# Kernel optimization log

Hardware: AMD Instinct MI355X
Metric: run time of the kernel (lower is better)

Reference implementation:

```python
import jax, jax.numpy as jnp
import numpy as np

V, MAXLEN, D, I, C, L, S = 32000, 4096, 1024, 4096, 1024, 4, 4096


def setup_inputs() -> dict:
    key = jax.random.key(0)
    ks = jax.random.split(key, 20)
    sd = 0.02
    inp = {
        "input_indices": jax.random.randint(ks[0], (S,), 0, V),
        "emb": jax.random.normal(ks[1], (V, D), jnp.float32) * sd,
        "pos": jax.random.normal(ks[2], (MAXLEN, D), jnp.float32) * sd,
        "Wq": jax.random.normal(ks[3], (L, D, I), jnp.float32) * sd,
        "bq": jnp.zeros((L, I), jnp.float32),
        "Wk": jax.random.normal(ks[4], (L, D, I), jnp.float32) * sd,
        "bk": jnp.zeros((L, I), jnp.float32),
        "Wv": jax.random.normal(ks[5], (L, D, I), jnp.float32) * sd,
        "bv": jnp.zeros((L, I), jnp.float32),
        "Wo": jax.random.normal(ks[6], (L, I, D), jnp.float32) * sd,
        "bo": jnp.zeros((L, D), jnp.float32),
        "W1": jax.random.normal(ks[7], (L, D, I), jnp.float32) * sd,
        "b1": jnp.zeros((L, I), jnp.float32),
        "W2": jax.random.normal(ks[8], (L, I, D), jnp.float32) * sd,
        "b2": jnp.zeros((L, D), jnp.float32),
        "Wout": jax.random.normal(ks[9], (D, C), jnp.float32) * sd,
        "bout": jnp.zeros((C,), jnp.float32),
    }
    return inp


def reference(input_indices, emb, pos, Wq, bq, Wk, bk, Wv, bv, Wo, bo, W1, b1, W2, b2, Wout, bout):
    s = input_indices.shape[0]
    x = emb[input_indices] + pos[:s]  # [S, D]
    causal_mask = jnp.triu(jnp.ones((s, s), bool), k=1)  # True above diagonal -> masked
    scale = 1.0 / np.sqrt(Wq.shape[-1]).astype(np.float32)

    def layer(x, p):
        wq, bq_, wk, bk_, wv, bv_, wo, bo_, w1, b1_, w2, b2_ = p
        q = x @ wq + bq_  # [S, I]
        k = x @ wk + bk_
        v = x @ wv + bv_
        scores = (q @ k.T) * scale  # [S, S]
        scores = jnp.where(causal_mask, -jnp.inf, scores)
        attn = jax.nn.softmax(scores, axis=-1)
        r = x + (attn @ v) @ wo + bo_  # residual + attention output projection
        f = jnp.maximum(r @ w1 + b1_, 0.0) @ w2 + b2_  # ReLU FFN
        return r + f, attn

    x, attention_maps = jax.lax.scan(
        layer, x, (Wq, bq, Wk, bk, Wv, bv, Wo, bo, W1, b1, W2, b2)
    )
    logits = x @ Wout + bout  # [S, C]
    log_probs = jax.nn.log_softmax(logits, axis=-1)
    return log_probs, attention_maps  # [S, C], [L, S, S]
```

## Files before the change

kernel.cpp:

```cpp
#include <hip/hip_runtime.h>
#include <stdint.h>
#include <math.h>

#define S_ 4096
#define D_ 1024
#define I_ 4096
#define C_ 1024
#define L_ 4

typedef unsigned short u16;
typedef short bf16x8 __attribute__((ext_vector_type(8)));
typedef float f32x4 __attribute__((ext_vector_type(4)));

__device__ __forceinline__ u16 f2bf(float f) {
  union { float f; uint32_t u; } c; c.f = f;
  return (u16)((c.u + 0x7FFFu + ((c.u >> 16) & 1u)) >> 16);
}
__device__ __forceinline__ float bf2f(u16 b) {
  union { uint32_t u; float f; } c; c.u = (uint32_t)b << 16;
  return c.f;
}
__device__ __forceinline__ u16 f2h(float f) {
  _Float16 h = (_Float16)f;
  return *(u16*)&h;
}
__device__ __forceinline__ float h2f(u16 b) {
  _Float16 h = *(_Float16*)&b;
  return (float)h;
}

__device__ __forceinline__ void gll16(const void* g, void* l) {
  __builtin_amdgcn_global_load_lds(
      (__attribute__((address_space(1))) void*)(g),
      (__attribute__((address_space(3))) void*)(l), 16, 0, 0);
}

#define BAR() asm volatile("s_barrier" ::: "memory")
#define WAITV(n) asm volatile("s_waitcnt vmcnt(" #n ")" ::: "memory")

__device__ __forceinline__ int xcd_swz(int orig, int nwg) {
  int q8 = nwg >> 3, r8 = nwg & 7;
  int xcd = orig & 7, rem = orig >> 3;
  return (xcd < r8 ? xcd * (q8 + 1) : r8 * (q8 + 1) + (xcd - r8) * q8) + rem;
}

__device__ __forceinline__ void gemm256_body(
    u16* sA, u16* sB,
    const u16* __restrict__ A, const u16* __restrict__ Bt,
    const float* __restrict__ bias,
    u16* __restrict__ outU, int isBF,
    u16* __restrict__ outT, int ldT,
    int N, int K, float scale, int relu,
    int row0, int col0, int t0, int t1)
{
  int tid = threadIdx.x, l = tid & 63;
  int w = tid >> 6;
  int wr = w >> 2, wc = w & 3;
  int lrow = l & 15, lq = l >> 4;
  int hb = wc >> 1;
  int rx = lrow & 7;

  const u16* ap[2]; const u16* bp[2]; int dst[2];
#pragma unroll
  for (int u = 0; u < 2; ++u) {
    int c = u * 512 + tid;
    int row = c >> 3;
    int oct = (c & 7) ^ (row & 7);
    ap[u] = A + (size_t)(row0 + row) * K + oct * 8;
    bp[u] = Bt + (size_t)(col0 + row) * K + oct * 8;
    dst[u] = c * 8;
  }

#define STAGE_A(par, hh, t)                                                     \
  { _Pragma("unroll") for (int u = 0; u < 2; ++u)                               \
      gll16(ap[u] + (size_t)(hh) * 128 * K + (t) * 64,                          \
            &sA[((par) * 2 + (hh)) * 8192 + dst[u]]); }
#define STAGE_B(par, hh, t)                                                     \
  { _Pragma("unroll") for (int u = 0; u < 2; ++u)                               \
      gll16(bp[u] + (size_t)(hh) * 128 * K + (t) * 64,                          \
            &sB[((par) * 2 + (hh)) * 8192 + dst[u]]); }
#define LD_A(DST, par, mh)                                                      \
  { _Pragma("unroll") for (int mi = 0; mi < 4; ++mi)                            \
    _Pragma("unroll") for (int kc = 0; kc < 2; ++kc)                            \
      DST[mi][kc] = *(const bf16x8*)&sA[((par) * 2 + wr) * 8192 +               \
          ((mh) * 64 + mi * 16 + lrow) * 64 + (((kc * 4 + lq) ^ rx) * 8)]; }
#define LD_B(DST, par, nh)                                                      \
  { _Pragma("unroll") for (int nj = 0; nj < 2; ++nj)                            \
    _Pragma("unroll") for (int kc = 0; kc < 2; ++kc)                            \
      DST[nj][kc] = *(const bf16x8*)&sB[((par) * 2 + hb) * 8192 +               \
          ((wc & 1) * 64 + (nh) * 32 + nj * 16 + lrow) * 64 +                   \
          (((kc * 4 + lq) ^ rx) * 8)]; }

  f32x4 acc[8][4];
#pragma unroll
  for (int i = 0; i < 8; ++i)
#pragma unroll
    for (int j = 0; j < 4; ++j) {
      acc[i][j][0] = 0.f; acc[i][j][1] = 0.f; acc[i][j][2] = 0.f; acc[i][j][3] = 0.f;
    }

#define MM(AF, MB, NB)                                                          \
  { __builtin_amdgcn_s_setprio(1);                                             \
    _Pragma("unroll") for (int kc = 0; kc < 2; ++kc)                            \
    _Pragma("unroll") for (int mi = 0; mi < 4; ++mi)                            \
    _Pragma("unroll") for (int nj = 0; nj < 2; ++nj)                            \
      acc[(MB) + mi][(NB) + nj] = __builtin_amdgcn_mfma_f32_16x16x32_bf16(      \
          AF[mi][kc], bfv[nj][kc], acc[(MB) + mi][(NB) + nj], 0, 0, 0);         \
    __builtin_amdgcn_s_setprio(0); }

  bf16x8 afA[4][2], afB[4][2], bfv[2][2];

  STAGE_A(0, 0, t0); STAGE_A(0, 1, t0); STAGE_B(0, 0, t0); STAGE_B(0, 1, t0);
  STAGE_A(1, 0, t0 + 1); STAGE_A(1, 1, t0 + 1); STAGE_B(1, 0, t0 + 1);
  WAITV(6);
  BAR();

  for (int t = t0; t < t1; ++t) {
    int p = (t - t0) & 1;
    LD_A(afA, p, 0);
    LD_B(bfv, p, 0);
    LD_A(afB, p, 1);
    if (t + 1 < t1) STAGE_B(p ^ 1, 1, t + 1);
    BAR();
    MM(afA, 0, 0);
    BAR();
    if (t + 2 < t1) STAGE_A(p, 0, t + 2);
    BAR();
    MM(afB, 4, 0);
    BAR();
    LD_B(bfv, p, 1);
    if (t + 2 < t1) STAGE_A(p, 1, t + 2);
    BAR();
    MM(afB, 4, 2);
    BAR();
    if (t + 2 < t1) STAGE_B(p, 0, t + 2);
    BAR();
    MM(afA, 0, 2);
    if (t + 2 < t1) { WAITV(6); } else { WAITV(0); }
    BAR();
  }
#undef STAGE_A
#undef STAGE_B
#undef LD_A
#undef LD_B
#undef MM

  float biasv[4] = {0.f, 0.f, 0.f, 0.f};
  if (bias) {
#pragma unroll
    for (int j = 0; j < 4; ++j) biasv[j] = bias[col0 + wc * 64 + j * 16 + lrow];
  }

  if (outT) {
    u16* tlds = sA;
    int myhalf = wc >> 1;
    int colb = tid >> 5;
    int sub = tid & 31;
#pragma unroll
    for (int half = 0; half < 2; ++half) {
      BAR();
      if (myhalf == half) {
#pragma unroll
        for (int i = 0; i < 8; ++i)
#pragma unroll
          for (int r = 0; r < 4; ++r)
#pragma unroll
            for (int j = 0; j < 4; ++j) {
              int cl = (wc * 64 + j * 16 + lrow) & 127;
              int rowl = wr * 128 + i * 16 + lq * 4 + r;
              tlds[cl * 264 + rowl] = f2bf(acc[i][j][r] + biasv[j]);
            }
      }
      BAR();
#pragma unroll
      for (int it = 0; it < 8; ++it) {
        int cl = it * 16 + colb;
        size_t gb = (size_t)(col0 + half * 128 + cl) * ldT + row0 + sub * 8;
        bf16x8 v = *(const bf16x8*)&tlds[cl * 264 + sub * 8];
        *(bf16x8*)&outT[gb] = v;
      }
    }
    return;
  }

  u16* tlds = sA;
  int rl0 = tid >> 5;
  int ch = tid & 31;
#pragma unroll
  for (int half = 0; half < 2; ++half) {
    BAR();
    if (wr == half) {
#pragma unroll
      for (int i = 0; i < 8; ++i)
#pragma unroll
        for (int r = 0; r < 4; ++r)
#pragma unroll
          for (int j = 0; j < 4; ++j) {
            int rowl = i * 16 + lq * 4 + r;
            int cl = wc * 64 + j * 16 + lrow;
            float v = acc[i][j][r] * scale + biasv[j];
            if (relu) v = fmaxf(v, 0.f);
            tlds[rowl * 264 + cl] = isBF ? f2bf(v) : f2h(v);
          }
    }
    BAR();
#pragma unroll
    for (int it = 0; it < 8; ++it) {
      int rowl = it * 16 + rl0;
      size_t gb = (size_t)(row0 + half * 128 + rowl) * N + col0 + ch * 8;
      bf16x8 v = *(const bf16x8*)&tlds[rowl * 264 + ch * 8];
      *(bf16x8*)&outU[gb] = v;
    }
  }
}

__global__ __launch_bounds__(512, 2) void gemm256k(
    const u16* __restrict__ A, const u16* __restrict__ Bt,
    const float* __restrict__ bias, u16* __restrict__ outB,
    int M, int N, int K, float scale, int flags, int k0, int k1)
{
  extern __shared__ char smem[];
  int wg = xcd_swz(blockIdx.x, gridDim.x);
  int nbx = N / 256;
  int br = wg / nbx, bc = wg % nbx;
  gemm256_body((u16*)smem, (u16*)smem + 32768, A, Bt, bias, outB, 1,
               nullptr, 0, N, K, scale, flags & 1, br * 256, bc * 256,
               k0 / 64, k1 / 64);
}

struct B3 { const float* b[3]; };
__global__ __launch_bounds__(512, 2) void gemm256_qkv(
    const u16* __restrict__ A, const u16* __restrict__ BtBase,
    B3 b3, u16* __restrict__ outQK, u16* __restrict__ vT, int K)
{
  extern __shared__ char smem[];
  int wg = xcd_swz(blockIdx.x, gridDim.x);
  int z = wg >> 8;
  int tile = wg & 255;
  int br = tile >> 4, bc = tile & 15;
  if (z < 2) {
    gemm256_body((u16*)smem, (u16*)smem + 32768, A,
                 BtBase + (size_t)z * I_ * D_, b3.b[z],
                 outQK + (size_t)z * S_ * I_, 1, nullptr, 0,
                 I_, K, 1.0f, 0, br * 256, bc * 256, 0, K / 64);
  } else {
    gemm256_body((u16*)smem, (u16*)smem + 32768, A,
                 BtBase + (size_t)2 * I_ * D_, b3.b[2],
                 nullptr, 1, vT, S_,
                 I_, K, 1.0f, 0, br * 256, bc * 256, 0, K / 64);
  }
}

__global__ __launch_bounds__(512, 2) void gemm256_tri3(
    const u16* __restrict__ A, const u16* __restrict__ Bt,
    u16* __restrict__ out0, u16* __restrict__ out1, u16* __restrict__ out2,
    int K, float scale)
{
  extern __shared__ char smem[];
  int wg = xcd_swz(blockIdx.x, gridDim.x);
  int ntri = gridDim.x / 3;
  int chunk = wg / ntri;
  int tile = wg - chunk * ntri;
  int br = (int)((sqrtf(8.0f * (float)tile + 1.0f) - 1.0f) * 0.5f);
  while ((br + 1) * (br + 2) / 2 <= tile) ++br;
  while (br * (br + 1) / 2 > tile) --br;
  int bc = tile - br * (br + 1) / 2;
  int t0 = (chunk == 0) ? 0 : (chunk == 1 ? 22 : 43);
  int t1 = (chunk == 0) ? 22 : (chunk == 1 ? 43 : 64);
  u16* o = (chunk == 0) ? out0 : (chunk == 1 ? out1 : out2);
  gemm256_body((u16*)smem, (u16*)smem + 32768, A, Bt, nullptr,
               o, 0, nullptr, 0,
               S_, K, scale, 0, br * 256, bc * 256, t0, t1);
}

__global__ __launch_bounds__(512, 2) void gemm256_pv(
    const u16* __restrict__ A, const u16* __restrict__ Bt,
    u16* __restrict__ outB, u16* __restrict__ pvH)
{
  extern __shared__ char smem[];
  int wg = xcd_swz(blockIdx.x, gridDim.x);
  if (wg < 128) {
    int br = wg >> 4, bc = wg & 15;
    gemm256_body((u16*)smem, (u16*)smem + 32768, A, Bt, nullptr,
                 outB, 1, nullptr, 0, I_, S_, 1.0f, 0,
                 br * 256, bc * 256, 0, (br + 1) * 4);
  } else {
    int c = wg - 128;
    int br = 8 + (c >> 5);
    int bc = (c >> 1) & 15;
    int chunk = c & 1;
    int lim = (br + 1) * 4;
    int half = lim >> 1;
    u16* o = pvH + (size_t)chunk * (S_ / 2) * I_ - (size_t)2048 * I_;
    gemm256_body((u16*)smem, (u16*)smem + 32768, A, Bt, nullptr,
                 o, 0, nullptr, 0, I_, S_, 1.0f, 0,
                 br * 256, bc * 256, chunk ? half : 0, chunk ? lim : half);
  }
}

__global__ __launch_bounds__(256) void combine2pv(
    const u16* __restrict__ pvH, u16* __restrict__ outB)
{
  const int MN = (S_ / 2) * I_;
  int i = (blockIdx.x * 256 + threadIdx.x) * 4;
  ushort4 a = *(const ushort4*)&pvH[i];
  ushort4 b = *(const ushort4*)&pvH[MN + i];
  ushort4 o;
  o.x = f2bf(h2f(a.x) + h2f(b.x));
  o.y = f2bf(h2f(a.y) + h2f(b.y));
  o.z = f2bf(h2f(a.z) + h2f(b.z));
  o.w = f2bf(h2f(a.w) + h2f(b.w));
  *(ushort4*)&outB[(size_t)2048 * I_ + i] = o;
}

__global__ __launch_bounds__(512, 2) void gemm256_ks4(
    const u16* __restrict__ A, const u16* __restrict__ Bt,
    u16* __restrict__ pOut, int M, int N, int K)
{
  extern __shared__ char smem[];
  int wg = xcd_swz(blockIdx.x, gridDim.x);
  int chunk = wg & 3;
  int tile = wg >> 2;
  int nbx = N / 256;
  int br = tile / nbx, bc = tile % nbx;
  u16* o = pOut + (size_t)chunk * M * N;
  int kq = K / 4;
  gemm256_body((u16*)smem, (u16*)smem + 32768, A, Bt, nullptr,
               o, 0, nullptr, 0, N, K, 1.0f, 0,
               br * 256, bc * 256, (chunk * kq) / 64, ((chunk + 1) * kq) / 64);
}

__global__ __launch_bounds__(256) void combine4(
    const u16* __restrict__ p, const float* __restrict__ bias,
    const u16* __restrict__ residB, u16* __restrict__ outB, int MN, int N)
{
  int i = (blockIdx.x * 256 + threadIdx.x) * 4;
  ushort4 a = *(const ushort4*)&p[i];
  ushort4 b = *(const ushort4*)&p[MN + i];
  ushort4 c = *(const ushort4*)&p[2 * MN + i];
  ushort4 d = *(const ushort4*)&p[3 * MN + i];
  ushort4 rb = *(const ushort4*)&residB[i];
  f32x4 v;
  v[0] = h2f(a.x) + h2f(b.x) + h2f(c.x) + h2f(d.x) + bf2f(rb.x);
  v[1] = h2f(a.y) + h2f(b.y) + h2f(c.y) + h2f(d.y) + bf2f(rb.y);
  v[2] = h2f(a.z) + h2f(b.z) + h2f(c.z) + h2f(d.z) + bf2f(rb.z);
  v[3] = h2f(a.w) + h2f(b.w) + h2f(c.w) + h2f(d.w) + bf2f(rb.w);
  int col = i & (N - 1);
  v += *(const f32x4*)&bias[col];
  ushort4 o;
  o.x = f2bf(v[0]); o.y = f2bf(v[1]); o.z = f2bf(v[2]); o.w = f2bf(v[3]);
  *(ushort4*)&outB[i] = o;
}

struct T6 {
  const float* src[6];
  u16* dst[6];
};

__global__ __launch_bounds__(256) void trans6_f2b(T6 a) {
  __shared__ float tile[64][65];
  int z = blockIdx.z;
  bool big = (z == 3 || z == 5);
  int R = big ? I_ : D_;
  int C = big ? D_ : I_;
  int bid = blockIdx.y * gridDim.x + blockIdx.x;
  int nbx = C / 64;
  int bx = bid % nbx, by = bid / nbx;
  const float* src = a.src[z];
  u16* dst = a.dst[z];
  int c0 = bx * 64, r0 = by * 64;
  int tx = threadIdx.x & 63, ty = threadIdx.x >> 6;
#pragma unroll
  for (int i = 0; i < 64; i += 4)
    tile[ty + i][tx] = src[(size_t)(r0 + ty + i) * C + c0 + tx];
  __syncthreads();
#pragma unroll
  for (int i = 0; i < 64; i += 4)
    dst[(size_t)(c0 + ty + i) * R + r0 + tx] = f2bf(tile[tx][ty + i]);
}

__global__ __launch_bounds__(256) void trans_f2b(const float* __restrict__ src,
                                                 u16* __restrict__ dst, int R, int C)
{
  __shared__ float tile[32][33];
  int c0 = blockIdx.x * 32, r0 = blockIdx.y * 32;
  int tx = threadIdx.x & 31, ty = threadIdx.x >> 5;
#pragma unroll
  for (int i = 0; i < 32; i += 8)
    tile[ty + i][tx] = src[(size_t)(r0 + ty + i) * C + c0 + tx];
  __syncthreads();
#pragma unroll
  for (int i = 0; i < 32; i += 8)
    dst[(size_t)(c0 + ty + i) * R + r0 + tx] = f2bf(tile[tx][ty + i]);
}

__global__ __launch_bounds__(256) void embed_k(const int* __restrict__ idx,
                                               const float* __restrict__ emb,
                                               const float* __restrict__ pos,
                                               u16* __restrict__ xb)
{
  int i = (blockIdx.x * 256 + threadIdx.x) * 8;
  int s = i >> 10;
  int d = i & (D_ - 1);
  const float* e = emb + (size_t)idx[s] * D_ + d;
  const float* p = pos + (size_t)s * D_ + d;
  f32x4 v0 = *(const f32x4*)e + *(const f32x4*)p;
  f32x4 v1 = *(const f32x4*)(e + 4) + *(const f32x4*)(p + 4);
  ushort4 b0, b1;
  b0.x = f2bf(v0[0]); b0.y = f2bf(v0[1]); b0.z = f2bf(v0[2]); b0.w = f2bf(v0[3]);
  b1.x = f2bf(v1[0]); b1.y = f2bf(v1[1]); b1.z = f2bf(v1[2]); b1.w = f2bf(v1[3]);
  *(ushort4*)&xb[i] = b0;
  *(ushort4*)&xb[i + 4] = b1;
}

__global__ __launch_bounds__(256) void softmax_causal(float* __restrict__ att,
                                                      const u16* __restrict__ p0,
                                                      const u16* __restrict__ p1,
                                                      const u16* __restrict__ p2,
                                                      u16* __restrict__ attB)
{
  int s = blockIdx.x;
  __shared__ float row[S_];
  __shared__ float red[8];
  int tid = threadIdx.x, l = tid & 63, w = tid >> 6;
  int nv = s + 1;
  size_t base = (size_t)s * S_;
  float m = -3.0e38f;
  for (int c = tid; c < nv; c += 256) {
    float v = h2f(p0[base + c]) + h2f(p1[base + c]) + h2f(p2[base + c]);
    row[c] = v; m = fmaxf(m, v);
  }
#pragma unroll
  for (int off = 32; off; off >>= 1) m = fmaxf(m, __shfl_xor(m, off, 64));
  if (l == 0) red[w] = m;
  __syncthreads();
  m = fmaxf(fmaxf(red[0], red[1]), fmaxf(red[2], red[3]));
  float sum = 0.f;
  for (int c = tid; c < nv; c += 256) { float e = __expf(row[c] - m); row[c] = e; sum += e; }
#pragma unroll
  for (int off = 32; off; off >>= 1) sum += __shfl_xor(sum, off, 64);
  if (l == 0) red[4 + w] = sum;
  __syncthreads();
  sum = red[4] + red[5] + red[6] + red[7];
  float inv = 1.0f / sum;
  int nb = ((s >> 8) + 1) * 256;
  for (int c = tid; c < S_; c += 256) {
    float p = (c < nv) ? row[c] * inv : 0.0f;
    att[base + c] = p;
    if (c < nb) attB[base + c] = f2bf(p);
  }
}

__global__ __launch_bounds__(256) void logsoftmax_k(const u16* __restrict__ p,
                                                    const float* __restrict__ bias,
                                                    float* __restrict__ out)
{
  const int MN = S_ * C_;
  int s = blockIdx.x;
  int tid = threadIdx.x, l = tid & 63, w = tid >> 6;
  __shared__ float red[8];
  size_t base = (size_t)s * C_;
  float v[4];
  float m = -3.0e38f;
#pragma unroll
  for (int k = 0; k < 4; ++k) {
    int col = tid + k * 256;
    size_t i = base + col;
    v[k] = h2f(p[i]) + h2f(p[MN + i]) + h2f(p[2 * MN + i]) + h2f(p[3 * MN + i])
           + bias[col];
    m = fmaxf(m, v[k]);
  }
#pragma unroll
  for (int off = 32; off; off >>= 1) m = fmaxf(m, __shfl_xor(m, off, 64));
  if (l == 0) red[w] = m;
  __syncthreads();
  m = fmaxf(fmaxf(red[0], red[1]), fmaxf(red[2], red[3]));
  float sum = 0.f;
#pragma unroll
  for (int k = 0; k < 4; ++k) sum += __expf(v[k] - m);
#pragma unroll
  for (int off = 32; off; off >>= 1) sum += __shfl_xor(sum, off, 64);
  if (l == 0) red[4 + w] = sum;
  __syncthreads();
  sum = red[4] + red[5] + red[6] + red[7];
  float lz = logf(sum);
#pragma unroll
  for (int k = 0; k < 4; ++k) out[base + tid + k * 256] = v[k] - m - lz;
}

extern "C" void kernel_launch(void* const* d_in, const int* in_sizes, int n_in,
                              void* d_out, int out_size, void* d_ws, size_t ws_size,
                              hipStream_t stream) {
  (void)in_sizes; (void)n_in; (void)out_size; (void)ws_size;
  const int*   idx  = (const int*)d_in[0];
  const float* emb  = (const float*)d_in[1];
  const float* pos  = (const float*)d_in[2];
  const float* Wq   = (const float*)d_in[3];
  const float* bq   = (const float*)d_in[4];
  const float* Wk   = (const float*)d_in[5];
  const float* bk   = (const float*)d_in[6];
  const float* Wv   = (const float*)d_in[7];
  const float* bv   = (const float*)d_in[8];
  const float* Wo   = (const float*)d_in[9];
  const float* bo   = (const float*)d_in[10];
  const float* W1   = (const float*)d_in[11];
  const float* b1   = (const float*)d_in[12];
  const float* W2   = (const float*)d_in[13];
  const float* b2   = (const float*)d_in[14];
  const float* Wout = (const float*)d_in[15];
  const float* bout = (const float*)d_in[16];
  float* out = (float*)d_out;

  char* ws = (char*)d_ws;
  const size_t MB = 1024ull * 1024ull;
  u16*  xbf    = (u16*)(ws + 16 * MB);
  u16*  bufQ   = (u16*)(ws + 24 * MB);
  u16*  bufK   = (u16*)(ws + 56 * MB);
  u16*  bufVT  = (u16*)(ws + 120 * MB);
  u16*  attnB  = (u16*)(ws + 152 * MB);
  u16* WqT   = (u16*)(ws + 200 * MB);
  u16* WkT   = (u16*)(ws + 208 * MB);
  u16* WvT   = (u16*)(ws + 216 * MB);
  u16* WoT   = (u16*)(ws + 224 * MB);
  u16* W1T   = (u16*)(ws + 232 * MB);
  u16* W2T   = (u16*)(ws + 240 * MB);
  u16* WoutT = (u16*)(ws + 248 * MB);
  u16* attP0 = (u16*)(ws + 256 * MB);
  u16* attP1 = (u16*)(ws + 288 * MB);
  u16* attP2 = (u16*)(ws + 320 * MB);
  u16* shP   = (u16*)(ws + 352 * MB);

  const float iscale = 1.0f / 64.0f;
  const int LDSB = 131072;
  hipFuncSetAttribute((const void*)gemm256k,
                      hipFuncAttributeMaxDynamicSharedMemorySize, LDSB);
  hipFuncSetAttribute((const void*)gemm256_qkv,
                      hipFuncAttributeMaxDynamicSharedMemorySize, LDSB);
  hipFuncSetAttribute((const void*)gemm256_tri3,
                      hipFuncAttributeMaxDynamicSharedMemorySize, LDSB);
  hipFuncSetAttribute((const void*)gemm256_pv,
                      hipFuncAttributeMaxDynamicSharedMemorySize, LDSB);
  hipFuncSetAttribute((const void*)gemm256_ks4,
                      hipFuncAttributeMaxDynamicSharedMemorySize, LDSB);
  const int G_SQ = (S_ / 256) * (I_ / 256);

  embed_k<<<(S_ * D_) / (256 * 8), 256, 0, stream>>>(idx, emb, pos, xbf);

  for (int layer = 0; layer < L_; ++layer) {
    T6 t6;
    t6.src[0] = Wq + (size_t)layer * D_ * I_; t6.dst[0] = WqT;
    t6.src[1] = Wk + (size_t)layer * D_ * I_; t6.dst[1] = WkT;
    t6.src[2] = Wv + (size_t)layer * D_ * I_; t6.dst[2] = WvT;
    t6.src[3] = Wo + (size_t)layer * I_ * D_; t6.dst[3] = WoT;
    t6.src[4] = W1 + (size_t)layer * D_ * I_; t6.dst[4] = W1T;
    t6.src[5] = W2 + (size_t)layer * I_ * D_; t6.dst[5] = W2T;
    trans6_f2b<<<dim3(64, 16, 6), 256, 0, stream>>>(t6);

    B3 b3;
    b3.b[0] = bq + (size_t)layer * I_;
    b3.b[1] = bk + (size_t)layer * I_;
    b3.b[2] = bv + (size_t)layer * I_;
    gemm256_qkv<<<3 * G_SQ, 512, LDSB, stream>>>(xbf, WqT, b3, bufQ, bufVT, D_);

    float* attL = out + (size_t)S_ * C_ + (size_t)layer * S_ * S_;
    gemm256_tri3<<<3 * 136, 512, LDSB, stream>>>(bufQ, bufK, attP0, attP1, attP2,
                                                 I_, iscale);

    softmax_causal<<<S_, 256, 0, stream>>>(attL, attP0, attP1, attP2, attnB);

    gemm256_pv<<<384, 512, LDSB, stream>>>(attnB, bufVT, bufQ, shP);
    combine2pv<<<(S_ / 2) * (I_ / 1024), 256, 0, stream>>>(shP, bufQ);

    gemm256_ks4<<<(S_ / 256) * (D_ / 256) * 4, 512, LDSB, stream>>>(
        bufQ, WoT, shP, S_, D_, I_);
    combine4<<<(S_ * D_) / 1024, 256, 0, stream>>>(
        shP, bo + (size_t)layer * D_, xbf, xbf, S_ * D_, D_);

    gemm256k<<<G_SQ, 512, LDSB, stream>>>(
        xbf, W1T, b1 + (size_t)layer * I_, bufK,
        S_, I_, D_, 1.0f, 1, 0, D_);

    gemm256_ks4<<<(S_ / 256) * (D_ / 256) * 4, 512, LDSB, stream>>>(
        bufK, W2T, shP, S_, D_, I_);
    combine4<<<(S_ * D_) / 1024, 256, 0, stream>>>(
        shP, b2 + (size_t)layer * D_, xbf, xbf, S_ * D_, D_);
  }

  trans_f2b<<<dim3(C_ / 32, D_ / 32), 256, 0, stream>>>(Wout, WoutT, D_, C_);
  gemm256_ks4<<<(S_ / 256) * (C_ / 256) * 4, 512, LDSB, stream>>>(
      xbf, WoutT, shP, S_, C_, D_);
  logsoftmax_k<<<S_, 256, 0, stream>>>(shP, bout, out);
}
```

Baseline: 2.105 ms.

## Rebalance QK^T split-K into 4-way chunks, reorder PV tiles, fold Wout transpose

The causal QK^T kernel now splits most of the 136 triangular tiles four ways along K and the last 32 three ways, writing a fourth partial buffer. That buffer is zero-filled for the three-way tiles so the softmax can always sum four partials. This gives 512 workgroups instead of 408 to fill the GPU better, at the cost of an extra partial read in softmax and a small fill kernel. The PV kernel's tile ordering is reassigned so the heavy bottom rows are scheduled first, and the Wout transpose is merged into the first layer's weight-transpose launch.

```diff
diff --git a/kernel.cpp b/kernel.cpp
--- a/kernel.cpp
+++ b/kernel.cpp
@@ -42,6 +42,13 @@
   int q8 = nwg >> 3, r8 = nwg & 7;
   int xcd = orig & 7, rem = orig >> 3;
   return (xcd < r8 ? xcd * (q8 + 1) : r8 * (q8 + 1) + (xcd - r8) * q8) + rem;
+}
+
+__device__ __forceinline__ void tri_decode(int tidx, int& br, int& bc) {
+  br = (int)((sqrtf(8.0f * (float)tidx + 1.0f) - 1.0f) * 0.5f);
+  while ((br + 1) * (br + 2) / 2 <= tidx) ++br;
+  while (br * (br + 1) / 2 > tidx) --br;
+  bc = tidx - br * (br + 1) / 2;
 }
 
 __device__ __forceinline__ void gemm256_body(
@@ -251,44 +258,82 @@
   }
 }
 
-__global__ __launch_bounds__(512, 2) void gemm256_tri3(
+__global__ __launch_bounds__(512, 2) void gemm256_tri(
     const u16* __restrict__ A, const u16* __restrict__ Bt,
-    u16* __restrict__ out0, u16* __restrict__ out1, u16* __restrict__ out2,
-    int K, float scale)
+    u16* __restrict__ p0, u16* __restrict__ p1, u16* __restrict__ p2,
+    u16* __restrict__ p3, int K, float scale)
 {
   extern __shared__ char smem[];
   int wg = xcd_swz(blockIdx.x, gridDim.x);
-  int ntri = gridDim.x / 3;
-  int chunk = wg / ntri;
-  int tile = wg - chunk * ntri;
-  int br = (int)((sqrtf(8.0f * (float)tile + 1.0f) - 1.0f) * 0.5f);
-  while ((br + 1) * (br + 2) / 2 <= tile) ++br;
-  while (br * (br + 1) / 2 > tile) --br;
-  int bc = tile - br * (br + 1) / 2;
-  int t0 = (chunk == 0) ? 0 : (chunk == 1 ? 22 : 43);
-  int t1 = (chunk == 0) ? 22 : (chunk == 1 ? 43 : 64);
-  u16* o = (chunk == 0) ? out0 : (chunk == 1 ? out1 : out2);
+  int c32 = wg >> 5, off = wg & 31;
+  int tidx, t0, t1;
+  u16* o;
+  if (off < 6) {
+    int i3 = c32 * 6 + off;
+    tidx = 104 + i3 / 3;
+    int chk = i3 % 3;
+    t0 = (chk == 0) ? 0 : (chk == 1 ? 21 : 42);
+    t1 = (chk == 0) ? 21 : (chk == 1 ? 42 : 64);
+    o = (chk == 0) ? p0 : (chk == 1 ? p1 : p2);
+  } else {
+    int i4 = c32 * 26 + (off - 6);
+    tidx = i4 >> 2;
+    int chk = i4 & 3;
+    t0 = chk * 16; t1 = t0 + 16;
+    o = (chk == 0) ? p0 : (chk == 1 ? p1 : (chk == 2 ? p2 : p3));
+  }
+  int br, bc;
+  tri_decode(tidx, br, bc);
   gemm256_body((u16*)smem, (u16*)smem + 32768, A, Bt, nullptr,
                o, 0, nullptr, 0,
                S_, K, scale, 0, br * 256, bc * 256, t0, t1);
 }
 
+__global__ __launch_bounds__(256) void fillp3(u16* __restrict__ p3) {
+  int b = blockIdx.x;
+  int tidx = 104 + (b >> 5);
+  int br, bc;
+  tri_decode(tidx, br, bc);
+  int inner = b & 31;
+  int row = br * 256 + inner * 8 + (threadIdx.x >> 5);
+  int col = bc * 256 + (threadIdx.x & 31) * 8;
+  ushort4 z4 = {0, 0, 0, 0};
+  *(ushort4*)&p3[(size_t)row * S_ + col] = z4;
+  *(ushort4*)&p3[(size_t)row * S_ + col + 4] = z4;
+}
+
 __global__ __launch_bounds__(512, 2) void gemm256_pv(
     const u16* __restrict__ A, const u16* __restrict__ Bt,
     u16* __restrict__ outB, u16* __restrict__ pvH)
 {
   extern __shared__ char smem[];
   int wg = xcd_swz(blockIdx.x, gridDim.x);
-  if (wg < 128) {
-    int br = wg >> 4, bc = wg & 15;
+  int s0, br, dir;
+  if      (wg < 32)  { s0 = 0;   br = 15; dir = 0; }
+  else if (wg < 48)  { s0 = 32;  br = 7;  dir = 1; }
+  else if (wg < 80)  { s0 = 48;  br = 14; dir = 0; }
+  else if (wg < 112) { s0 = 80;  br = 13; dir = 0; }
+  else if (wg < 128) { s0 = 112; br = 6;  dir = 1; }
+  else if (wg < 160) { s0 = 128; br = 12; dir = 0; }
+  else if (wg < 192) { s0 = 160; br = 11; dir = 0; }
+  else if (wg < 208) { s0 = 192; br = 5;  dir = 1; }
+  else if (wg < 240) { s0 = 208; br = 10; dir = 0; }
+  else if (wg < 272) { s0 = 240; br = 9;  dir = 0; }
+  else if (wg < 288) { s0 = 272; br = 4;  dir = 1; }
+  else if (wg < 320) { s0 = 288; br = 8;  dir = 0; }
+  else if (wg < 336) { s0 = 320; br = 3;  dir = 1; }
+  else if (wg < 352) { s0 = 336; br = 2;  dir = 1; }
+  else if (wg < 368) { s0 = 352; br = 1;  dir = 1; }
+  else               { s0 = 368; br = 0;  dir = 1; }
+  int u = wg - s0;
+  if (dir) {
+    int bc = u;
     gemm256_body((u16*)smem, (u16*)smem + 32768, A, Bt, nullptr,
                  outB, 1, nullptr, 0, I_, S_, 1.0f, 0,
                  br * 256, bc * 256, 0, (br + 1) * 4);
   } else {
-    int c = wg - 128;
-    int br = 8 + (c >> 5);
-    int bc = (c >> 1) & 15;
-    int chunk = c & 1;
+    int bc = u >> 1;
+    int chunk = u & 1;
     int lim = (br + 1) * 4;
     int half = lim >> 1;
     u16* o = pvH + (size_t)chunk * (S_ / 2) * I_ - (size_t)2048 * I_;
@@ -352,19 +397,21 @@
   *(ushort4*)&outB[i] = o;
 }
 
-struct T6 {
-  const float* src[6];
-  u16* dst[6];
+struct T7 {
+  const float* src[7];
+  u16* dst[7];
 };
 
-__global__ __launch_bounds__(256) void trans6_f2b(T6 a) {
+__global__ __launch_bounds__(256) void trans7_f2b(T7 a) {
   __shared__ float tile[64][65];
   int z = blockIdx.z;
-  bool big = (z == 3 || z == 5);
-  int R = big ? I_ : D_;
-  int C = big ? D_ : I_;
+  int R, C;
+  if (z == 6) { R = D_; C = C_; }
+  else if (z == 3 || z == 5) { R = I_; C = D_; }
+  else { R = D_; C = I_; }
   int bid = blockIdx.y * gridDim.x + blockIdx.x;
   int nbx = C / 64;
+  if (bid >= nbx * (R / 64)) return;
   int bx = bid % nbx, by = bid / nbx;
   const float* src = a.src[z];
   u16* dst = a.dst[z];
@@ -376,21 +423,6 @@
   __syncthreads();
 #pragma unroll
   for (int i = 0; i < 64; i += 4)
-    dst[(size_t)(c0 + ty + i) * R + r0 + tx] = f2bf(tile[tx][ty + i]);
-}
-
-__global__ __launch_bounds__(256) void trans_f2b(const float* __restrict__ src,
-                                                 u16* __restrict__ dst, int R, int C)
-{
-  __shared__ float tile[32][33];
-  int c0 = blockIdx.x * 32, r0 = blockIdx.y * 32;
-  int tx = threadIdx.x & 31, ty = threadIdx.x >> 5;
-#pragma unroll
-  for (int i = 0; i < 32; i += 8)
-    tile[ty + i][tx] = src[(size_t)(r0 + ty + i) * C + c0 + tx];
-  __syncthreads();
-#pragma unroll
-  for (int i = 0; i < 32; i += 8)
     dst[(size_t)(c0 + ty + i) * R + r0 + tx] = f2bf(tile[tx][ty + i]);
 }
 
@@ -417,6 +449,7 @@
                                                       const u16* __restrict__ p0,
                                                       const u16* __restrict__ p1,
                                                       const u16* __restrict__ p2,
+                                                      const u16* __restrict__ p3,
                                                       u16* __restrict__ attB)
 {
   int s = blockIdx.x;
@@ -427,7 +460,8 @@
   size_t base = (size_t)s * S_;
   float m = -3.0e38f;
   for (int c = tid; c < nv; c += 256) {
-    float v = h2f(p0[base + c]) + h2f(p1[base + c]) + h2f(p2[base + c]);
+    float v = h2f(p0[base + c]) + h2f(p1[base + c]) + h2f(p2[base + c])
+            + h2f(p3[base + c]);
     row[c] = v; m = fmaxf(m, v);
   }
 #pragma unroll
@@ -536,7 +570,7 @@
                       hipFuncAttributeMaxDynamicSharedMemorySize, LDSB);
   hipFuncSetAttribute((const void*)gemm256_qkv,
                       hipFuncAttributeMaxDynamicSharedMemorySize, LDSB);
-  hipFuncSetAttribute((const void*)gemm256_tri3,
+  hipFuncSetAttribute((const void*)gemm256_tri,
                       hipFuncAttributeMaxDynamicSharedMemorySize, LDSB);
   hipFuncSetAttribute((const void*)gemm256_pv,
                       hipFuncAttributeMaxDynamicSharedMemorySize, LDSB);
@@ -547,14 +581,15 @@
   embed_k<<<(S_ * D_) / (256 * 8), 256, 0, stream>>>(idx, emb, pos, xbf);
 
   for (int layer = 0; layer < L_; ++layer) {
-    T6 t6;
-    t6.src[0] = Wq + (size_t)layer * D_ * I_; t6.dst[0] = WqT;
-    t6.src[1] = Wk + (size_t)layer * D_ * I_; t6.dst[1] = WkT;
-    t6.src[2] = Wv + (size_t)layer * D_ * I_; t6.dst[2] = WvT;
-    t6.src[3] = Wo + (size_t)layer * I_ * D_; t6.dst[3] = WoT;
-    t6.src[4] = W1 + (size_t)layer * D_ * I_; t6.dst[4] = W1T;
-    t6.src[5] = W2 + (size_t)layer * I_ * D_; t6.dst[5] = W2T;
-    trans6_f2b<<<dim3(64, 16, 6), 256, 0, stream>>>(t6);
+    T7 t7;
+    t7.src[0] = Wq + (size_t)layer * D_ * I_; t7.dst[0] = WqT;
+    t7.src[1] = Wk + (size_t)layer * D_ * I_; t7.dst[1] = WkT;
+    t7.src[2] = Wv + (size_t)layer * D_ * I_; t7.dst[2] = WvT;
+    t7.src[3] = Wo + (size_t)layer * I_ * D_; t7.dst[3] = WoT;
+    t7.src[4] = W1 + (size_t)layer * D_ * I_; t7.dst[4] = W1T;
+    t7.src[5] = W2 + (size_t)layer * I_ * D_; t7.dst[5] = W2T;
+    t7.src[6] = Wout;                         t7.dst[6] = WoutT;
+    trans7_f2b<<<dim3(64, 16, layer == 0 ? 7 : 6), 256, 0, stream>>>(t7);
 
     B3 b3;
     b3.b[0] = bq + (size_t)layer * I_;
@@ -562,11 +597,12 @@
     b3.b[2] = bv + (size_t)layer * I_;
     gemm256_qkv<<<3 * G_SQ, 512, LDSB, stream>>>(xbf, WqT, b3, bufQ, bufVT, D_);
 
+    fillp3<<<1024, 256, 0, stream>>>(shP);
+    gemm256_tri<<<512, 512, LDSB, stream>>>(bufQ, bufK, attP0, attP1, attP2,
+                                            shP, I_, iscale);
+
     float* attL = out + (size_t)S_ * C_ + (size_t)layer * S_ * S_;
-    gemm256_tri3<<<3 * 136, 512, LDSB, stream>>>(bufQ, bufK, attP0, attP1, attP2,
-                                                 I_, iscale);
-
-    softmax_causal<<<S_, 256, 0, stream>>>(attL, attP0, attP1, attP2, attnB);
+    softmax_causal<<<S_, 256, 0, stream>>>(attL, attP0, attP1, attP2, shP, attnB);
 
     gemm256_pv<<<384, 512, LDSB, stream>>>(attnB, bufVT, bufQ, shP);
     combine2pv<<<(S_ / 2) * (I_ / 1024), 256, 0, stream>>>(shP, bufQ);
@@ -586,7 +622,6 @@
         shP, b2 + (size_t)layer * D_, xbf, xbf, S_ * D_, D_);
   }
 
-  trans_f2b<<<dim3(C_ / 32, D_ / 32), 256, 0, stream>>>(Wout, WoutT, D_, C_);
   gemm256_ks4<<<(S_ / 256) * (C_ / 256) * 4, 512, LDSB, stream>>>(
       xbf, WoutT, shP, S_, C_, D_);
   logsoftmax_k<<<S_, 256, 0, stream>>>(shP, bout, out);
```

After: 2.090 ms. Within noise of the previous version (-0.7%).
